# Kernel tuning notes

Measured on AMD Instinct MI355X. Metric: run time of the kernel, lower is better.

Reference implementation:

```python
import jax, jax.numpy as jnp
import numpy as np

EPS = 0.1
MAX_ITER = 10
SIGMA = 0.1
NEG_INF = -1e8


def gaussian_position_filter(in_size, out_size, dtype):
    a = jnp.arange(0.0, in_size, dtype=dtype)[:, None] / in_size
    b = jnp.arange(0.0, out_size, dtype=dtype)[None, :] / out_size
    return jnp.exp(-(((a - b) / SIGMA) ** 2))[None]


def log_sinkhorn(K, mask, max_iter):
    # K: n x in_size x out_size (already scaled by 1/eps); mask: n x in_size bool
    n, in_size, out_size = K.shape
    dt = K.dtype
    loga = jnp.log((out_size / mask.sum(1, keepdims=True)).astype(dt))  # n x 1

    def neg_lse(u, v, axis):
        Z = K + u[:, :, None] + v[:, None, :]
        return -jax.nn.logsumexp(Z, axis=axis)

    def body(carry, _):
        u, v = carry
        u = loga + neg_lse(u, v, -1)           # row update: n x in_size
        u = jnp.where(mask, u, jnp.asarray(NEG_INF, dt))
        v = neg_lse(u, v, 1)                   # col update: n x out_size
        return (u, v), None

    u0 = jnp.zeros((n, in_size), dt)
    v0 = jnp.zeros((n, out_size), dt)
    (u, v), _ = jax.lax.scan(body, (u0, v0), None, length=max_iter)
    return jnp.exp(K + u[:, :, None] + v[:, None, :])  # transport plan T


def setup_inputs() -> dict:
    key = jax.random.key(0)
    k1, k2, k3 = jax.random.split(key, 3)
    B, S, O, D = 16, 4096, 512, 128
    return {
        "input": jax.random.normal(k1, (B, S, D), jnp.float32),
        "target": jax.random.normal(k2, (B, O, D), jnp.float32),
        "iou_cost": jax.random.uniform(k3, (B, S, O), jnp.float32),
        "mask": jnp.ones((B, S), jnp.bool_),
    }


def reference(input, target, iou_cost, mask):
    # input: B x S x D, target: B x O x D, iou_cost: B x S x O, mask: B x S
    B, S, D = input.shape
    O = target.shape[1]
    pf = gaussian_position_filter(S, O, input.dtype)
    K = jnp.einsum('bsd,bod->bso', input, target) - iou_cost  # similarity minus IoU cost
    K = pf * K / EPS
    T = pf * log_sinkhorn(K, mask, MAX_ITER) * S              # B x S x O
    # output: B x (out_size*heads) x in_size, heads=1
    return jnp.transpose(T, (0, 2, 1)).reshape(B, O, S)
```

## Files before the change

### kernel.cpp

```cpp
#include <hip/hip_runtime.h>
#include <hip/hip_bf16.h>

#define B_ 16
#define S_ 4096
#define O_ 512
#define D_ 128
#define NEG_INF_ -1e8f
#define MAX_ITER_ 10
#define YST 513

typedef __attribute__((ext_vector_type(8))) short short8;
typedef __attribute__((ext_vector_type(4))) float floatx4;
typedef __attribute__((ext_vector_type(4))) unsigned short ushort4v;

__device__ inline unsigned short f32_to_bf16_rne(float x) {
    union { float f; unsigned int u; } c; c.f = x;
    unsigned int u = c.u;
    unsigned int r = (u + 0x7FFFu + ((u >> 16) & 1u)) >> 16;
    return (unsigned short)r;
}
__device__ inline float bf16_bits_to_f32(unsigned short h) {
    union { unsigned int u; float f; } c; c.u = ((unsigned int)h) << 16;
    return c.f;
}
__device__ inline void gload_lds16(const float* g, float* l) {
    __builtin_amdgcn_global_load_lds((const __attribute__((address_space(1))) void*)g,
                                     (__attribute__((address_space(3))) void*)l, 16, 0, 0);
}

__global__ void init_kernel(const int* __restrict__ mask,
                            float* __restrict__ u, float* __restrict__ v,
                            float* __restrict__ loga) {
    __shared__ int sc[256];
    int b = blockIdx.x, t = threadIdx.x;
    int c = 0;
    for (int k = t; k < S_; k += 256) c += (mask[(size_t)b * S_ + k] != 0);
    sc[t] = c; __syncthreads();
    for (int st = 128; st > 0; st >>= 1) { if (t < st) sc[t] += sc[t + st]; __syncthreads(); }
    if (t == 0) loga[b] = logf((float)O_ / (float)sc[0]);
    for (int k = t; k < S_; k += 256) u[(size_t)b * S_ + k] = 0.f;
    for (int k = t; k < O_; k += 256) v[b * O_ + k] = 0.f;
}

__global__ __launch_bounds__(256) void split_kernel(const float* __restrict__ src,
                                                    unsigned short* __restrict__ hi,
                                                    unsigned short* __restrict__ lo, int n4) {
    int i = blockIdx.x * 256 + threadIdx.x;
    if (i >= n4) return;
    float4 x = ((const float4*)src)[i];
    float xs[4] = {x.x, x.y, x.z, x.w};
    ushort4v h, l;
#pragma unroll
    for (int j = 0; j < 4; ++j) {
        unsigned short hh = f32_to_bf16_rne(xs[j]);
        float rem = xs[j] - bf16_bits_to_f32(hh);
        h[j] = hh; l[j] = f32_to_bf16_rne(rem);
    }
    ((ushort4v*)hi)[i] = h;
    ((ushort4v*)lo)[i] = l;
}

__global__ __launch_bounds__(256) void gemm_nat(const unsigned short* __restrict__ in_hi,
                                                const unsigned short* __restrict__ in_lo,
                                                const unsigned short* __restrict__ tg_hi,
                                                const unsigned short* __restrict__ tg_lo,
                                                const float* __restrict__ iou,
                                                float* __restrict__ K) {
    __shared__ float siou[128 * 64];
    int b = blockIdx.z;
    int s0 = blockIdx.x * 128;
    int o0 = blockIdx.y * 64;
    int t = threadIdx.x, wid = t >> 6, lane = t & 63, fr = lane & 15, kg = lane >> 4;

#pragma unroll
    for (int i = 0; i < 8; ++i) {
        int ii = wid * 8 + i;
        int row = ii * 4 + (lane >> 4);
        int col = (((lane & 15) + (row & 15)) & 15) * 4;
        const float* g = iou + ((size_t)b * S_ + s0 + row) * O_ + o0 + col;
        gload_lds16(g, &siou[ii * 256]);
    }

    const unsigned short* ih = in_hi + ((size_t)b * S_ + s0 + wid * 32 + fr) * D_;
    const unsigned short* il = in_lo + ((size_t)b * S_ + s0 + wid * 32 + fr) * D_;
    const unsigned short* th = tg_hi + ((size_t)b * O_ + o0 + fr) * D_;
    const unsigned short* tl = tg_lo + ((size_t)b * O_ + o0 + fr) * D_;

    floatx4 acc[2][4];
#pragma unroll
    for (int i = 0; i < 2; ++i)
#pragma unroll
        for (int j = 0; j < 4; ++j) acc[i][j] = (floatx4){0.f, 0.f, 0.f, 0.f};

#pragma unroll
    for (int kb = 0; kb < 4; ++kb) {
        int ko = kb * 32 + kg * 8;
        short8 T_h[4], T_l[4];
#pragma unroll
        for (int j = 0; j < 4; ++j) {
            T_h[j] = *(const short8*)(th + (size_t)j * 16 * D_ + ko);
            T_l[j] = *(const short8*)(tl + (size_t)j * 16 * D_ + ko);
        }
#pragma unroll
        for (int i = 0; i < 2; ++i) {
            short8 I_h = *(const short8*)(ih + (size_t)i * 16 * D_ + ko);
            short8 I_l = *(const short8*)(il + (size_t)i * 16 * D_ + ko);
#pragma unroll
            for (int j = 0; j < 4; ++j) {
                acc[i][j] = __builtin_amdgcn_mfma_f32_16x16x32_bf16(T_l[j], I_h, acc[i][j], 0, 0, 0);
                acc[i][j] = __builtin_amdgcn_mfma_f32_16x16x32_bf16(T_h[j], I_l, acc[i][j], 0, 0, 0);
                acc[i][j] = __builtin_amdgcn_mfma_f32_16x16x32_bf16(T_h[j], I_h, acc[i][j], 0, 0, 0);
            }
        }
    }
    __syncthreads();

#pragma unroll
    for (int i = 0; i < 2; ++i) {
        int rowl = wid * 32 + i * 16 + fr;
        int s = s0 + rowl;
        float sn = (float)s * (1.0f / S_);
        size_t rowb = ((size_t)b * S_ + s) * O_;
#pragma unroll
        for (int j = 0; j < 4; ++j) {
            int obl = j * 16 + kg * 4;
            int x = (obl - fr * 4) & 63;
            float4 iv = *(const float4*)&siou[rowl * 64 + x];
            float ivs[4] = {iv.x, iv.y, iv.z, iv.w};
            float tmp[4];
#pragma unroll
            for (int r = 0; r < 4; ++r) {
                float d = sn - (float)(o0 + obl + r) * (1.0f / O_);
                float pf = __expf(-100.0f * d * d);
                tmp[r] = pf * (acc[i][j][r] - ivs[r]) * 10.0f;
            }
            float4 q; q.x = tmp[0]; q.y = tmp[1]; q.z = tmp[2]; q.w = tmp[3];
            *(float4*)(K + rowb + o0 + obl) = q;
        }
    }
}

template <int FIRST>
__global__ __launch_bounds__(256) void sink_iter(const float* __restrict__ K,
                                                 const float* __restrict__ vin,
                                                 float* __restrict__ u,
                                                 float2* __restrict__ colma,
                                                 const int* __restrict__ mask,
                                                 const float* __restrict__ loga) {
    __shared__ float sv[O_];
    __shared__ float sy[16 * YST];
    int b = blockIdx.y;
    int t = threadIdx.x, fr = t & 15, sl = t >> 4;
    if (!FIRST) {
        for (int i = t; i < O_; i += 256) sv[i] = vin[b * O_ + i];
        __syncthreads();
    }
    int sbase = blockIdx.x * 64;
    float lg = loga[b];
    float Mc0 = -INFINITY, Ac0 = 0.f, Mc1 = -INFINITY, Ac1 = 0.f;

    float bufA[32], bufB[32];
    auto loadK = [&](float (&dst)[32], int tau) {
        const float* krow = K + ((size_t)b * S_ + sbase + tau * 16 + sl) * O_ + fr * 4;
#pragma unroll
        for (int k = 0; k < 8; ++k) {
            float4 q = *(const float4*)(krow + k * 64);
            dst[k * 4 + 0] = q.x; dst[k * 4 + 1] = q.y;
            dst[k * 4 + 2] = q.z; dst[k * 4 + 3] = q.w;
        }
    };
    auto process = [&](float (&cur)[32], float (&nxt)[32], int tau, bool pre) {
        int s = sbase + tau * 16 + sl;
        size_t srow = (size_t)b * S_ + s;
        float uold = FIRST ? 0.f : u[srow];
        int mk = mask[srow];
        if (pre) loadK(nxt, tau + 1);

        float xv[32];
        if (FIRST) {
#pragma unroll
            for (int i = 0; i < 32; ++i) xv[i] = cur[i];
        } else {
#pragma unroll
            for (int k = 0; k < 8; ++k) {
                float4 vvq = *(const float4*)&sv[fr * 4 + k * 64];
                xv[k * 4 + 0] = cur[k * 4 + 0] + uold + vvq.x;
                xv[k * 4 + 1] = cur[k * 4 + 1] + uold + vvq.y;
                xv[k * 4 + 2] = cur[k * 4 + 2] + uold + vvq.z;
                xv[k * 4 + 3] = cur[k * 4 + 3] + uold + vvq.w;
            }
        }
        float M = -INFINITY;
#pragma unroll
        for (int i = 0; i < 32; ++i) M = fmaxf(M, xv[i]);
#pragma unroll
        for (int off = 1; off < 16; off <<= 1) M = fmaxf(M, __shfl_xor(M, off));
        float a = 0.f;
#pragma unroll
        for (int i = 0; i < 32; ++i) a += __expf(xv[i] - M);
#pragma unroll
        for (int off = 1; off < 16; off <<= 1) a += __shfl_xor(a, off);
        float unew = lg - (M + logf(a));
        if (!mk) unew = NEG_INF_;
        if (fr == 0) u[srow] = unew;

        float c = unew - uold;
#pragma unroll
        for (int k = 0; k < 8; ++k) {
            float4 q;
            q.x = xv[k * 4 + 0] + c; q.y = xv[k * 4 + 1] + c;
            q.z = xv[k * 4 + 2] + c; q.w = xv[k * 4 + 3] + c;
            *(float4*)&sy[sl * YST + fr * 4 + k * 64] = q;
        }
        __syncthreads();
#pragma unroll
        for (int h = 0; h < 2; ++h) {
            int o = t + h * 256;
            float q[16];
            float m = -INFINITY;
#pragma unroll
            for (int r = 0; r < 16; ++r) { q[r] = sy[r * YST + o]; m = fmaxf(m, q[r]); }
            float aa = 0.f;
#pragma unroll
            for (int r = 0; r < 16; ++r) aa += __expf(q[r] - m);
            float Mo = h ? Mc1 : Mc0, Ao = h ? Ac1 : Ac0;
            float nm = fmaxf(Mo, m);
            Ao = Ao * __expf(Mo - nm) + aa * __expf(m - nm);
            if (h) { Mc1 = nm; Ac1 = Ao; } else { Mc0 = nm; Ac0 = Ao; }
        }
        __syncthreads();
    };
    loadK(bufA, 0);
    process(bufA, bufB, 0, true);
    process(bufB, bufA, 1, true);
    process(bufA, bufB, 2, true);
    process(bufB, bufA, 3, false);

    float2* cout = colma + ((size_t)b * 64 + blockIdx.x) * O_;
    {
        float2 r0; r0.x = Mc0; r0.y = Ac0;
        cout[t] = r0;
        float2 r1; r1.x = Mc1; r1.y = Ac1;
        cout[t + 256] = r1;
    }
}

__global__ __launch_bounds__(256) void finalize_v(const float2* __restrict__ colma,
                                                  float* __restrict__ v) {
    __shared__ float sm[4][64], sa[4][64];
    int b = blockIdx.y;
    int ol = threadIdx.x & 63, cg = threadIdx.x >> 6;
    int o = blockIdx.x * 64 + ol;
    const float2* cp = colma + (size_t)b * 64 * O_ + o;
    float M = -INFINITY, A = 0.f;
#pragma unroll 4
    for (int i = 0; i < 16; ++i) {
        float2 q = cp[(size_t)(cg * 16 + i) * O_];
        float nm = fmaxf(M, q.x);
        A = A * __expf(M - nm) + q.y * __expf(q.x - nm);
        M = nm;
    }
    sm[cg][ol] = M; sa[cg][ol] = A;
    __syncthreads();
    if (threadIdx.x < 64) {
        M = sm[0][ol]; A = sa[0][ol];
#pragma unroll
        for (int i = 1; i < 4; ++i) {
            float mi = sm[i][ol], ai = sa[i][ol];
            float nm = fmaxf(M, mi);
            A = A * __expf(M - nm) + ai * __expf(mi - nm);
            M = nm;
        }
        v[b * O_ + o] = -(M + logf(A));
    }
}

__global__ __launch_bounds__(256) void final_tr(const float* __restrict__ K,
                                                const float* __restrict__ u,
                                                const float* __restrict__ v,
                                                float* __restrict__ out) {
    __shared__ float tile[64][65];
    __shared__ float su[64], svv[64];
    int b = blockIdx.z;
    int s0 = blockIdx.x * 64, o0 = blockIdx.y * 64;
    int t = threadIdx.x, fr = t & 15, rg = t >> 4;
    if (t < 64) su[t] = u[(size_t)b * S_ + s0 + t];
    else if (t < 128) svv[t - 64] = v[b * O_ + o0 + t - 64];
    __syncthreads();
#pragma unroll
    for (int p = 0; p < 4; ++p) {
        int sl = p * 16 + rg;
        int s = s0 + sl;
        float4 x = *(const float4*)(K + ((size_t)b * S_ + s) * O_ + o0 + fr * 4);
        float us = su[sl];
        float sn = (float)s * (1.0f / S_);
        float xs[4] = {x.x, x.y, x.z, x.w};
#pragma unroll
        for (int c = 0; c < 4; ++c) {
            int ol = fr * 4 + c;
            float d = sn - (float)(o0 + ol) * (1.0f / O_);
            tile[ol][sl] = 4096.0f * __expf(xs[c] + us + svv[ol] - 100.0f * d * d);
        }
    }
    __syncthreads();
#pragma unroll
    for (int p = 0; p < 4; ++p) {
        int ol = p * 16 + rg;
        float4 y;
        y.x = tile[ol][fr * 4 + 0];
        y.y = tile[ol][fr * 4 + 1];
        y.z = tile[ol][fr * 4 + 2];
        y.w = tile[ol][fr * 4 + 3];
        *(float4*)(out + ((size_t)b * O_ + o0 + ol) * S_ + s0 + fr * 4) = y;
    }
}


__global__ __launch_bounds__(256) void gemm_kt2(const unsigned short* __restrict__ in_hi,
                                                const unsigned short* __restrict__ in_lo,
                                                const unsigned short* __restrict__ tg_hi,
                                                const unsigned short* __restrict__ tg_lo,
                                                const float* __restrict__ iou,
                                                float* __restrict__ KT) {
    __shared__ float siou[64 * 65];
    int b = blockIdx.z;
    int s0 = blockIdx.x * 64;
    int o0 = blockIdx.y * 64;
    int t = threadIdx.x;
    {
        const float* ir = iou + ((size_t)b * S_ + s0 + (t >> 2)) * O_ + o0 + (t & 3) * 16;
        float4 q0 = ((const float4*)ir)[0];
        float4 q1 = ((const float4*)ir)[1];
        float4 q2 = ((const float4*)ir)[2];
        float4 q3 = ((const float4*)ir)[3];
        float* dst = &siou[(t >> 2) * 65 + (t & 3) * 16];
        dst[0]=q0.x; dst[1]=q0.y; dst[2]=q0.z; dst[3]=q0.w;
        dst[4]=q1.x; dst[5]=q1.y; dst[6]=q1.z; dst[7]=q1.w;
        dst[8]=q2.x; dst[9]=q2.y; dst[10]=q2.z; dst[11]=q2.w;
        dst[12]=q3.x; dst[13]=q3.y; dst[14]=q3.z; dst[15]=q3.w;
    }
    int w = t >> 6, lane = t & 63, fr = lane & 15, kg = lane >> 4;
    const unsigned short* ta_hi = tg_hi + ((size_t)b * O_ + o0 + w * 16 + fr) * D_;
    const unsigned short* ta_lo = tg_lo + ((size_t)b * O_ + o0 + w * 16 + fr) * D_;
    const unsigned short* ib_hi = in_hi + ((size_t)b * S_ + s0 + fr) * D_;
    const unsigned short* ib_lo = in_lo + ((size_t)b * S_ + s0 + fr) * D_;
    floatx4 acc[4];
#pragma unroll
    for (int st = 0; st < 4; ++st) acc[st] = (floatx4){0.f, 0.f, 0.f, 0.f};
#pragma unroll
    for (int kb = 0; kb < 4; ++kb) {
        int ko = kb * 32 + kg * 8;
        short8 ah = *(const short8*)(ta_hi + ko);
        short8 al2 = *(const short8*)(ta_lo + ko);
#pragma unroll
        for (int st = 0; st < 4; ++st) {
            short8 bh2 = *(const short8*)(ib_hi + (size_t)st * 16 * D_ + ko);
            short8 bl2 = *(const short8*)(ib_lo + (size_t)st * 16 * D_ + ko);
            acc[st] = __builtin_amdgcn_mfma_f32_16x16x32_bf16(al2, bh2, acc[st], 0, 0, 0);
            acc[st] = __builtin_amdgcn_mfma_f32_16x16x32_bf16(ah, bl2, acc[st], 0, 0, 0);
            acc[st] = __builtin_amdgcn_mfma_f32_16x16x32_bf16(ah, bh2, acc[st], 0, 0, 0);
        }
    }
    __syncthreads();
#pragma unroll
    for (int st = 0; st < 4; ++st) {
        int s = s0 + st * 16 + fr;
        float ds = (float)s * (1.0f / S_);
#pragma unroll
        for (int r = 0; r < 4; ++r) {
            int o = o0 + w * 16 + kg * 4 + r;
            float d = ds - (float)o * (1.0f / O_);
            float pf = __expf(-100.0f * d * d);
            float iouv = siou[(st * 16 + fr) * 65 + (w * 16 + kg * 4 + r)];
            KT[((size_t)b * O_ + o) * S_ + s] = pf * (acc[st][r] - iouv) * 10.0f;
        }
    }
}

__global__ __launch_bounds__(256) void row_update2(const float* __restrict__ KT,
                                                   const float* __restrict__ v,
                                                   float* __restrict__ u,
                                                   const int* __restrict__ mask,
                                                   const float* __restrict__ loga) {
    __shared__ float sv[O_];
    __shared__ float lm[4][128], la[4][128];
    int b = blockIdx.y;
    int s0 = blockIdx.x * 128;
    int t = threadIdx.x, lane = t & 63, w = t >> 6;
    for (int i = t; i < O_; i += 256) sv[i] = v[b * O_ + i];
    __syncthreads();
    const float* kt = KT + (size_t)b * O_ * S_ + s0 + lane * 2;
    float m0 = -INFINITY, m1 = -INFINITY, a0 = 0.f, a1 = 0.f;
    int ob = w * 128;
#pragma unroll 8
    for (int i = 0; i < 128; ++i) {
        int o = ob + i;
        float2 x2 = *(const float2*)(kt + (size_t)o * S_);
        float vo = sv[o];
        float x0 = x2.x + vo, x1 = x2.y + vo;
        if (x0 > m0) { a0 = a0 * __expf(m0 - x0) + 1.f; m0 = x0; } else a0 += __expf(x0 - m0);
        if (x1 > m1) { a1 = a1 * __expf(m1 - x1) + 1.f; m1 = x1; } else a1 += __expf(x1 - m1);
    }
    lm[w][lane * 2] = m0;     la[w][lane * 2] = a0;
    lm[w][lane * 2 + 1] = m1; la[w][lane * 2 + 1] = a1;
    __syncthreads();
    if (t < 128) {
        float M = lm[0][t], A = la[0][t];
#pragma unroll
        for (int i = 1; i < 4; ++i) {
            float mi = lm[i][t], ai = la[i][t];
            float nm = fmaxf(M, mi);
            A = A * __expf(M - nm) + ai * __expf(mi - nm);
            M = nm;
        }
        float lse = M + logf(A);
        size_t si = (size_t)b * S_ + s0 + t;
        u[si] = mask[si] ? (loga[b] - u[si] - lse) : NEG_INF_;
    }
}

template <int FIN>
__global__ __launch_bounds__(256) void col_update2(float* __restrict__ KT,
                                                   const float* __restrict__ u,
                                                   float* __restrict__ v) {
    __shared__ float red[8];
    int b = blockIdx.y, o = blockIdx.x;
    int t = threadIdx.x;
    float* kt = KT + ((size_t)b * O_ + o) * S_;
    const float* ub = u + (size_t)b * S_;
    float vold = v[b * O_ + o];
    float xs[16];
    float m = -INFINITY, a = 0.f;
#pragma unroll
    for (int k = 0; k < 4; ++k) {
        int s = k * 1024 + t * 4;
        float4 kx = *(const float4*)(kt + s);
        float4 ux = *(const float4*)(ub + s);
        float x0 = kx.x + ux.x, x1 = kx.y + ux.y, x2 = kx.z + ux.z, x3 = kx.w + ux.w;
        if (FIN) { xs[k*4] = x0; xs[k*4+1] = x1; xs[k*4+2] = x2; xs[k*4+3] = x3; }
        float cm = fmaxf(fmaxf(x0, x1), fmaxf(x2, x3));
        float nm = fmaxf(m, cm);
        a = a * __expf(m - nm) + __expf(x0 - nm) + __expf(x1 - nm)
                               + __expf(x2 - nm) + __expf(x3 - nm);
        m = nm;
    }
#pragma unroll
    for (int off = 1; off < 64; off <<= 1) {
        float mo = __shfl_xor(m, off), ao = __shfl_xor(a, off);
        float nm = fmaxf(m, mo);
        a = a * __expf(m - nm) + ao * __expf(mo - nm);
        m = nm;
    }
    int w = t >> 6;
    if ((t & 63) == 0) { red[w * 2] = m; red[w * 2 + 1] = a; }
    __syncthreads();
    float M = red[0], A = red[1];
#pragma unroll
    for (int i = 1; i < 4; ++i) {
        float mi = red[i * 2], ai = red[i * 2 + 1];
        float nm = fmaxf(M, mi);
        A = A * __expf(M - nm) + ai * __expf(mi - nm);
        M = nm;
    }
    float lse = M + logf(A);
    float vn = -vold - lse;
    if (t == 0) v[b * O_ + o] = vn;
    if (FIN) {
        float oo = (float)o * (1.0f / O_);
#pragma unroll
        for (int k = 0; k < 4; ++k) {
            int s = k * 1024 + t * 4;
            float4 r;
            float rr[4];
#pragma unroll
            for (int j = 0; j < 4; ++j) {
                float d = (float)(s + j) * (1.0f / S_) - oo;
                rr[j] = 4096.0f * __expf(xs[k * 4 + j] + vn - 100.0f * d * d);
            }
            r.x = rr[0]; r.y = rr[1]; r.z = rr[2]; r.w = rr[3];
            *(float4*)(kt + s) = r;
        }
    }
}


extern "C" void kernel_launch(void* const* d_in, const int* in_sizes, int n_in,
                              void* d_out, int out_size, void* d_ws, size_t ws_size,
                              hipStream_t stream) {
    const float* input  = (const float*)d_in[0];
    const float* target = (const float*)d_in[1];
    const float* iou    = (const float*)d_in[2];
    const int*   mask   = (const int*)d_in[3];
    float* out = (float*)d_out;
    float* wsf = (float*)d_ws;

    const size_t N_IN = (size_t)B_ * S_ * D_;
    const size_t N_TG = (size_t)B_ * O_ * D_;
    const size_t NK   = (size_t)B_ * S_ * O_;

    float* u    = wsf;
    float* v    = u + (size_t)B_ * S_;
    float* loga = v + (size_t)B_ * O_;

    float* Knat = loga + 16;
    float* region = Knat + NK;
    unsigned short* f_in_hi = (unsigned short*)region;
    unsigned short* f_in_lo = f_in_hi + N_IN;
    unsigned short* f_tg_hi = f_in_lo + N_IN;
    unsigned short* f_tg_lo = f_tg_hi + N_TG;
    float2* colma = (float2*)region;
    size_t need_fast = (size_t)((char*)(f_tg_lo + N_TG) - (char*)d_ws);

    unsigned short* m_in_hi = (unsigned short*)(loga + 16);
    unsigned short* m_in_lo = m_in_hi + N_IN;
    unsigned short* m_tg_hi = m_in_lo + N_IN;
    unsigned short* m_tg_lo = m_tg_hi + N_TG;
    size_t need_mid = (size_t)((char*)(m_tg_lo + N_TG) - (char*)d_ws);

    init_kernel<<<B_, 256, 0, stream>>>(mask, u, v, loga);

    if (ws_size >= need_fast) {
        split_kernel<<<(int)(N_IN / 4 / 256), 256, 0, stream>>>(input, f_in_hi, f_in_lo, (int)(N_IN / 4));
        split_kernel<<<(int)(N_TG / 4 / 256), 256, 0, stream>>>(target, f_tg_hi, f_tg_lo, (int)(N_TG / 4));
        gemm_nat<<<dim3(S_ / 128, O_ / 64, B_), 256, 0, stream>>>(f_in_hi, f_in_lo, f_tg_hi, f_tg_lo, iou, Knat);
        for (int it = 0; it < MAX_ITER_; ++it) {
            if (it == 0)
                sink_iter<1><<<dim3(S_ / 64, B_), 256, 0, stream>>>(Knat, v, u, colma, mask, loga);
            else
                sink_iter<0><<<dim3(S_ / 64, B_), 256, 0, stream>>>(Knat, v, u, colma, mask, loga);
            finalize_v<<<dim3(O_ / 64, B_), 256, 0, stream>>>(colma, v);
        }
        final_tr<<<dim3(S_ / 64, O_ / 64, B_), 256, 0, stream>>>(Knat, u, v, out);
    } else if (ws_size >= need_mid) {
        split_kernel<<<(int)(N_IN / 4 / 256), 256, 0, stream>>>(input, m_in_hi, m_in_lo, (int)(N_IN / 4));
        split_kernel<<<(int)(N_TG / 4 / 256), 256, 0, stream>>>(target, m_tg_hi, m_tg_lo, (int)(N_TG / 4));
        gemm_kt2<<<dim3(S_ / 64, O_ / 64, B_), 256, 0, stream>>>(m_in_hi, m_in_lo, m_tg_hi, m_tg_lo, iou, out);
        for (int it = 0; it < MAX_ITER_; ++it) {
            row_update2<<<dim3(S_ / 128, B_), 256, 0, stream>>>(out, v, u, mask, loga);
            if (it < MAX_ITER_ - 1)
                col_update2<0><<<dim3(O_, B_), 256, 0, stream>>>(out, u, v);
            else
                col_update2<1><<<dim3(O_, B_), 256, 0, stream>>>(out, u, v);
        }
    }
}
```

Measured before the change: 518.7 us.

## Fuse column finalize into sinkhorn iteration via last-block atomic; enlarge GEMM tile

Removes the separate finalize_v launch each iteration: every sink_iter block bumps a per-batch, per-iteration atomic counter, and the last of the 64 blocks merges the column max/sum partials and writes v. This cuts ten kernel launches but makes the final merge serial inside a single block per batch. Separately, the GEMM tile grows from 128 to 256 rows per block, with four 16-row tiles per wave instead of two. The iou tile is now read straight from global memory instead of being staged through LDS with global_load_lds.

```diff
diff --git a/kernel.cpp b/kernel.cpp
--- a/kernel.cpp
+++ b/kernel.cpp
@@ -23,14 +23,10 @@
     union { unsigned int u; float f; } c; c.u = ((unsigned int)h) << 16;
     return c.f;
 }
-__device__ inline void gload_lds16(const float* g, float* l) {
-    __builtin_amdgcn_global_load_lds((const __attribute__((address_space(1))) void*)g,
-                                     (__attribute__((address_space(3))) void*)l, 16, 0, 0);
-}
 
 __global__ void init_kernel(const int* __restrict__ mask,
                             float* __restrict__ u, float* __restrict__ v,
-                            float* __restrict__ loga) {
+                            float* __restrict__ loga, int* __restrict__ cnt) {
     __shared__ int sc[256];
     int b = blockIdx.x, t = threadIdx.x;
     int c = 0;
@@ -40,6 +36,7 @@
     if (t == 0) loga[b] = logf((float)O_ / (float)sc[0]);
     for (int k = t; k < S_; k += 256) u[(size_t)b * S_ + k] = 0.f;
     for (int k = t; k < O_; k += 256) v[b * O_ + k] = 0.f;
+    if (t < 160) cnt[t] = 0;
 }
 
 __global__ __launch_bounds__(256) void split_kernel(const float* __restrict__ src,
@@ -66,29 +63,19 @@
                                                 const unsigned short* __restrict__ tg_lo,
                                                 const float* __restrict__ iou,
                                                 float* __restrict__ K) {
-    __shared__ float siou[128 * 64];
     int b = blockIdx.z;
-    int s0 = blockIdx.x * 128;
+    int s0 = blockIdx.x * 256;
     int o0 = blockIdx.y * 64;
     int t = threadIdx.x, wid = t >> 6, lane = t & 63, fr = lane & 15, kg = lane >> 4;
 
-#pragma unroll
-    for (int i = 0; i < 8; ++i) {
-        int ii = wid * 8 + i;
-        int row = ii * 4 + (lane >> 4);
-        int col = (((lane & 15) + (row & 15)) & 15) * 4;
-        const float* g = iou + ((size_t)b * S_ + s0 + row) * O_ + o0 + col;
-        gload_lds16(g, &siou[ii * 256]);
-    }
-
-    const unsigned short* ih = in_hi + ((size_t)b * S_ + s0 + wid * 32 + fr) * D_;
-    const unsigned short* il = in_lo + ((size_t)b * S_ + s0 + wid * 32 + fr) * D_;
+    const unsigned short* ih = in_hi + ((size_t)b * S_ + s0 + wid * 64 + fr) * D_;
+    const unsigned short* il = in_lo + ((size_t)b * S_ + s0 + wid * 64 + fr) * D_;
     const unsigned short* th = tg_hi + ((size_t)b * O_ + o0 + fr) * D_;
     const unsigned short* tl = tg_lo + ((size_t)b * O_ + o0 + fr) * D_;
 
-    floatx4 acc[2][4];
-#pragma unroll
-    for (int i = 0; i < 2; ++i)
+    floatx4 acc[4][4];
+#pragma unroll
+    for (int i = 0; i < 4; ++i)
 #pragma unroll
         for (int j = 0; j < 4; ++j) acc[i][j] = (floatx4){0.f, 0.f, 0.f, 0.f};
 
@@ -102,7 +89,7 @@
             T_l[j] = *(const short8*)(tl + (size_t)j * 16 * D_ + ko);
         }
 #pragma unroll
-        for (int i = 0; i < 2; ++i) {
+        for (int i = 0; i < 4; ++i) {
             short8 I_h = *(const short8*)(ih + (size_t)i * 16 * D_ + ko);
             short8 I_l = *(const short8*)(il + (size_t)i * 16 * D_ + ko);
 #pragma unroll
@@ -113,46 +100,45 @@
             }
         }
     }
-    __syncthreads();
-
-#pragma unroll
-    for (int i = 0; i < 2; ++i) {
-        int rowl = wid * 32 + i * 16 + fr;
-        int s = s0 + rowl;
+
+#pragma unroll
+    for (int i = 0; i < 4; ++i) {
+        int s = s0 + wid * 64 + i * 16 + fr;
         float sn = (float)s * (1.0f / S_);
         size_t rowb = ((size_t)b * S_ + s) * O_;
 #pragma unroll
         for (int j = 0; j < 4; ++j) {
-            int obl = j * 16 + kg * 4;
-            int x = (obl - fr * 4) & 63;
-            float4 iv = *(const float4*)&siou[rowl * 64 + x];
+            int ob = o0 + j * 16 + kg * 4;
+            float4 iv = *(const float4*)(iou + rowb + ob);
             float ivs[4] = {iv.x, iv.y, iv.z, iv.w};
             float tmp[4];
 #pragma unroll
             for (int r = 0; r < 4; ++r) {
-                float d = sn - (float)(o0 + obl + r) * (1.0f / O_);
+                float d = sn - (float)(ob + r) * (1.0f / O_);
                 float pf = __expf(-100.0f * d * d);
                 tmp[r] = pf * (acc[i][j][r] - ivs[r]) * 10.0f;
             }
             float4 q; q.x = tmp[0]; q.y = tmp[1]; q.z = tmp[2]; q.w = tmp[3];
-            *(float4*)(K + rowb + o0 + obl) = q;
+            *(float4*)(K + rowb + ob) = q;
         }
     }
 }
 
 template <int FIRST>
 __global__ __launch_bounds__(256) void sink_iter(const float* __restrict__ K,
-                                                 const float* __restrict__ vin,
+                                                 float* __restrict__ v,
                                                  float* __restrict__ u,
                                                  float2* __restrict__ colma,
                                                  const int* __restrict__ mask,
-                                                 const float* __restrict__ loga) {
+                                                 const float* __restrict__ loga,
+                                                 int* __restrict__ cnt, int itIdx) {
     __shared__ float sv[O_];
     __shared__ float sy[16 * YST];
+    __shared__ int lastFlag;
     int b = blockIdx.y;
     int t = threadIdx.x, fr = t & 15, sl = t >> 4;
     if (!FIRST) {
-        for (int i = t; i < O_; i += 256) sv[i] = vin[b * O_ + i];
+        for (int i = t; i < O_; i += 256) sv[i] = v[b * O_ + i];
         __syncthreads();
     }
     int sbase = blockIdx.x * 64;
@@ -243,35 +229,28 @@
         float2 r1; r1.x = Mc1; r1.y = Ac1;
         cout[t + 256] = r1;
     }
-}
-
-__global__ __launch_bounds__(256) void finalize_v(const float2* __restrict__ colma,
-                                                  float* __restrict__ v) {
-    __shared__ float sm[4][64], sa[4][64];
-    int b = blockIdx.y;
-    int ol = threadIdx.x & 63, cg = threadIdx.x >> 6;
-    int o = blockIdx.x * 64 + ol;
-    const float2* cp = colma + (size_t)b * 64 * O_ + o;
-    float M = -INFINITY, A = 0.f;
-#pragma unroll 4
-    for (int i = 0; i < 16; ++i) {
-        float2 q = cp[(size_t)(cg * 16 + i) * O_];
-        float nm = fmaxf(M, q.x);
-        A = A * __expf(M - nm) + q.y * __expf(q.x - nm);
-        M = nm;
-    }
-    sm[cg][ol] = M; sa[cg][ol] = A;
-    __syncthreads();
-    if (threadIdx.x < 64) {
-        M = sm[0][ol]; A = sa[0][ol];
-#pragma unroll
-        for (int i = 1; i < 4; ++i) {
-            float mi = sm[i][ol], ai = sa[i][ol];
-            float nm = fmaxf(M, mi);
-            A = A * __expf(M - nm) + ai * __expf(mi - nm);
-            M = nm;
-        }
-        v[b * O_ + o] = -(M + logf(A));
+
+    __threadfence();
+    if (t == 0) {
+        int old = atomicAdd(&cnt[itIdx * 16 + b], 1);
+        lastFlag = (old == 63);
+    }
+    __syncthreads();
+    if (lastFlag) {
+        __threadfence();
+        const float2* cp0 = colma + ((size_t)b * 64) * O_;
+#pragma unroll
+        for (int h = 0; h < 2; ++h) {
+            int o = t + h * 256;
+            float M = -INFINITY, A = 0.f;
+            for (int c2 = 0; c2 < 64; ++c2) {
+                float2 q = cp0[(size_t)c2 * O_ + o];
+                float nm = fmaxf(M, q.x);
+                A = A * __expf(M - nm) + q.y * __expf(q.x - nm);
+                M = nm;
+            }
+            v[b * O_ + o] = -(M + logf(A));
+        }
     }
 }
 
@@ -501,8 +480,9 @@
     float* u    = wsf;
     float* v    = u + (size_t)B_ * S_;
     float* loga = v + (size_t)B_ * O_;
-
-    float* Knat = loga + 16;
+    int*   cnt  = (int*)(loga + 16);
+
+    float* Knat = loga + 16 + 160;
     float* region = Knat + NK;
     unsigned short* f_in_hi = (unsigned short*)region;
     unsigned short* f_in_lo = f_in_hi + N_IN;
@@ -511,24 +491,23 @@
     float2* colma = (float2*)region;
     size_t need_fast = (size_t)((char*)(f_tg_lo + N_TG) - (char*)d_ws);
 
-    unsigned short* m_in_hi = (unsigned short*)(loga + 16);
+    unsigned short* m_in_hi = (unsigned short*)(loga + 16 + 160);
     unsigned short* m_in_lo = m_in_hi + N_IN;
     unsigned short* m_tg_hi = m_in_lo + N_IN;
     unsigned short* m_tg_lo = m_tg_hi + N_TG;
     size_t need_mid = (size_t)((char*)(m_tg_lo + N_TG) - (char*)d_ws);
 
-    init_kernel<<<B_, 256, 0, stream>>>(mask, u, v, loga);
+    init_kernel<<<B_, 256, 0, stream>>>(mask, u, v, loga, cnt);
 
     if (ws_size >= need_fast) {
         split_kernel<<<(int)(N_IN / 4 / 256), 256, 0, stream>>>(input, f_in_hi, f_in_lo, (int)(N_IN / 4));
         split_kernel<<<(int)(N_TG / 4 / 256), 256, 0, stream>>>(target, f_tg_hi, f_tg_lo, (int)(N_TG / 4));
-        gemm_nat<<<dim3(S_ / 128, O_ / 64, B_), 256, 0, stream>>>(f_in_hi, f_in_lo, f_tg_hi, f_tg_lo, iou, Knat);
+        gemm_nat<<<dim3(S_ / 256, O_ / 64, B_), 256, 0, stream>>>(f_in_hi, f_in_lo, f_tg_hi, f_tg_lo, iou, Knat);
         for (int it = 0; it < MAX_ITER_; ++it) {
             if (it == 0)
-                sink_iter<1><<<dim3(S_ / 64, B_), 256, 0, stream>>>(Knat, v, u, colma, mask, loga);
+                sink_iter<1><<<dim3(S_ / 64, B_), 256, 0, stream>>>(Knat, v, u, colma, mask, loga, cnt, it);
             else
-                sink_iter<0><<<dim3(S_ / 64, B_), 256, 0, stream>>>(Knat, v, u, colma, mask, loga);
-            finalize_v<<<dim3(O_ / 64, B_), 256, 0, stream>>>(colma, v);
+                sink_iter<0><<<dim3(S_ / 64, B_), 256, 0, stream>>>(Knat, v, u, colma, mask, loga, cnt, it);
         }
         final_tr<<<dim3(S_ / 64, O_ / 64, B_), 256, 0, stream>>>(Knat, u, v, out);
     } else if (ws_size >= need_mid) {
```

After: 1.638 ms. 216% more time.

## Merge split launches, double GEMM row tile, read IoU directly from global

Applied to the files above, without the earlier changes.

The two bf16 hi/lo split kernels become one launch covering both input and target. The GEMM tile doubles from 128 to 256 S-rows per block, so each wave computes 64 rows and reuses the loaded target fragments across more MFMAs. The LDS staging of the IoU tile via global_load_lds is removed, and the epilogue reads IoU straight from global memory. This cuts launch overhead and target reloads, but uses more accumulator registers, halves the GEMM grid, and gives up the asynchronous IoU prefetch.

```diff
diff --git a/kernel.cpp b/kernel.cpp
--- a/kernel.cpp
+++ b/kernel.cpp
@@ -22,10 +22,6 @@
 __device__ inline float bf16_bits_to_f32(unsigned short h) {
     union { unsigned int u; float f; } c; c.u = ((unsigned int)h) << 16;
     return c.f;
-}
-__device__ inline void gload_lds16(const float* g, float* l) {
-    __builtin_amdgcn_global_load_lds((const __attribute__((address_space(1))) void*)g,
-                                     (__attribute__((address_space(3))) void*)l, 16, 0, 0);
 }
 
 __global__ void init_kernel(const int* __restrict__ mask,
@@ -42,11 +38,17 @@
     for (int k = t; k < O_; k += 256) v[b * O_ + k] = 0.f;
 }
 
-__global__ __launch_bounds__(256) void split_kernel(const float* __restrict__ src,
-                                                    unsigned short* __restrict__ hi,
-                                                    unsigned short* __restrict__ lo, int n4) {
+__global__ __launch_bounds__(256) void split_kernel(const float* __restrict__ srcA,
+                                                    unsigned short* __restrict__ hiA,
+                                                    unsigned short* __restrict__ loA, int n4A,
+                                                    const float* __restrict__ srcB,
+                                                    unsigned short* __restrict__ hiB,
+                                                    unsigned short* __restrict__ loB, int n4B) {
     int i = blockIdx.x * 256 + threadIdx.x;
-    if (i >= n4) return;
+    const float* src; unsigned short* hi; unsigned short* lo;
+    if (i < n4A) { src = srcA; hi = hiA; lo = loA; }
+    else if (i < n4A + n4B) { i -= n4A; src = srcB; hi = hiB; lo = loB; }
+    else return;
     float4 x = ((const float4*)src)[i];
     float xs[4] = {x.x, x.y, x.z, x.w};
     ushort4v h, l;
@@ -66,29 +68,19 @@
                                                 const unsigned short* __restrict__ tg_lo,
                                                 const float* __restrict__ iou,
                                                 float* __restrict__ K) {
-    __shared__ float siou[128 * 64];
     int b = blockIdx.z;
-    int s0 = blockIdx.x * 128;
+    int s0 = blockIdx.x * 256;
     int o0 = blockIdx.y * 64;
     int t = threadIdx.x, wid = t >> 6, lane = t & 63, fr = lane & 15, kg = lane >> 4;
 
-#pragma unroll
-    for (int i = 0; i < 8; ++i) {
-        int ii = wid * 8 + i;
-        int row = ii * 4 + (lane >> 4);
-        int col = (((lane & 15) + (row & 15)) & 15) * 4;
-        const float* g = iou + ((size_t)b * S_ + s0 + row) * O_ + o0 + col;
-        gload_lds16(g, &siou[ii * 256]);
-    }
-
-    const unsigned short* ih = in_hi + ((size_t)b * S_ + s0 + wid * 32 + fr) * D_;
-    const unsigned short* il = in_lo + ((size_t)b * S_ + s0 + wid * 32 + fr) * D_;
+    const unsigned short* ih = in_hi + ((size_t)b * S_ + s0 + wid * 64 + fr) * D_;
+    const unsigned short* il = in_lo + ((size_t)b * S_ + s0 + wid * 64 + fr) * D_;
     const unsigned short* th = tg_hi + ((size_t)b * O_ + o0 + fr) * D_;
     const unsigned short* tl = tg_lo + ((size_t)b * O_ + o0 + fr) * D_;
 
-    floatx4 acc[2][4];
-#pragma unroll
-    for (int i = 0; i < 2; ++i)
+    floatx4 acc[4][4];
+#pragma unroll
+    for (int i = 0; i < 4; ++i)
 #pragma unroll
         for (int j = 0; j < 4; ++j) acc[i][j] = (floatx4){0.f, 0.f, 0.f, 0.f};
 
@@ -102,7 +94,7 @@
             T_l[j] = *(const short8*)(tl + (size_t)j * 16 * D_ + ko);
         }
 #pragma unroll
-        for (int i = 0; i < 2; ++i) {
+        for (int i = 0; i < 4; ++i) {
             short8 I_h = *(const short8*)(ih + (size_t)i * 16 * D_ + ko);
             short8 I_l = *(const short8*)(il + (size_t)i * 16 * D_ + ko);
 #pragma unroll
@@ -113,29 +105,26 @@
             }
         }
     }
-    __syncthreads();
-
-#pragma unroll
-    for (int i = 0; i < 2; ++i) {
-        int rowl = wid * 32 + i * 16 + fr;
-        int s = s0 + rowl;
+
+#pragma unroll
+    for (int i = 0; i < 4; ++i) {
+        int s = s0 + wid * 64 + i * 16 + fr;
         float sn = (float)s * (1.0f / S_);
         size_t rowb = ((size_t)b * S_ + s) * O_;
 #pragma unroll
         for (int j = 0; j < 4; ++j) {
-            int obl = j * 16 + kg * 4;
-            int x = (obl - fr * 4) & 63;
-            float4 iv = *(const float4*)&siou[rowl * 64 + x];
+            int ob = o0 + j * 16 + kg * 4;
+            float4 iv = *(const float4*)(iou + rowb + ob);
             float ivs[4] = {iv.x, iv.y, iv.z, iv.w};
             float tmp[4];
 #pragma unroll
             for (int r = 0; r < 4; ++r) {
-                float d = sn - (float)(o0 + obl + r) * (1.0f / O_);
+                float d = sn - (float)(ob + r) * (1.0f / O_);
                 float pf = __expf(-100.0f * d * d);
                 tmp[r] = pf * (acc[i][j][r] - ivs[r]) * 10.0f;
             }
             float4 q; q.x = tmp[0]; q.y = tmp[1]; q.z = tmp[2]; q.w = tmp[3];
-            *(float4*)(K + rowb + o0 + obl) = q;
+            *(float4*)(K + rowb + ob) = q;
         }
     }
 }
@@ -520,9 +509,10 @@
     init_kernel<<<B_, 256, 0, stream>>>(mask, u, v, loga);
 
     if (ws_size >= need_fast) {
-        split_kernel<<<(int)(N_IN / 4 / 256), 256, 0, stream>>>(input, f_in_hi, f_in_lo, (int)(N_IN / 4));
-        split_kernel<<<(int)(N_TG / 4 / 256), 256, 0, stream>>>(target, f_tg_hi, f_tg_lo, (int)(N_TG / 4));
-        gemm_nat<<<dim3(S_ / 128, O_ / 64, B_), 256, 0, stream>>>(f_in_hi, f_in_lo, f_tg_hi, f_tg_lo, iou, Knat);
+        int n4A = (int)(N_IN / 4), n4B = (int)(N_TG / 4);
+        split_kernel<<<(n4A + n4B + 255) / 256, 256, 0, stream>>>(
+            input, f_in_hi, f_in_lo, n4A, target, f_tg_hi, f_tg_lo, n4B);
+        gemm_nat<<<dim3(S_ / 256, O_ / 64, B_), 256, 0, stream>>>(f_in_hi, f_in_lo, f_tg_hi, f_tg_lo, iou, Knat);
         for (int it = 0; it < MAX_ITER_; ++it) {
             if (it == 0)
                 sink_iter<1><<<dim3(S_ / 64, B_), 256, 0, stream>>>(Knat, v, u, colma, mask, loga);
@@ -532,8 +522,9 @@
         }
         final_tr<<<dim3(S_ / 64, O_ / 64, B_), 256, 0, stream>>>(Knat, u, v, out);
     } else if (ws_size >= need_mid) {
-        split_kernel<<<(int)(N_IN / 4 / 256), 256, 0, stream>>>(input, m_in_hi, m_in_lo, (int)(N_IN / 4));
-        split_kernel<<<(int)(N_TG / 4 / 256), 256, 0, stream>>>(target, m_tg_hi, m_tg_lo, (int)(N_TG / 4));
+        int n4A = (int)(N_IN / 4), n4B = (int)(N_TG / 4);
+        split_kernel<<<(n4A + n4B + 255) / 256, 256, 0, stream>>>(
+            input, m_in_hi, m_in_lo, n4A, target, m_tg_hi, m_tg_lo, n4B);
         gemm_kt2<<<dim3(S_ / 64, O_ / 64, B_), 256, 0, stream>>>(m_in_hi, m_in_lo, m_tg_hi, m_tg_lo, iou, out);
         for (int it = 0; it < MAX_ITER_; ++it) {
             row_update2<<<dim3(S_ / 128, B_), 256, 0, stream>>>(out, v, u, mask, loga);
```

Result: no change. 512.0 us (-1.3%).
